# Optimization experiments

Measured on AMD Instinct MI355X. Metric: run time of the kernel, lower is better.

The kernel has to match this reference:

```python
import jax, jax.numpy as jnp
import numpy as np

D_MODEL = 192
NODE_NUM = 64
DEPTH = 2
ALPHA = 0.05
NUM_LAYERS = 2
LN_EPS = 1e-5


def _gcn(x, p):
    # x: [N, in_dim*D_MODEL]; faithful port of GCN.forward (eval mode)
    nv1, nv2, ws, bs, wm, bm, we, be, wl, bl, g, b = p
    N = x.shape[0]
    in_dim = x.shape[1] // D_MODEL
    adp = jax.nn.softmax(jax.nn.relu(nv1 @ nv2), axis=1)            # [V,V]
    adj = adp + jnp.eye(NODE_NUM, dtype=x.dtype)
    a = adj / adj.sum(1, keepdims=True)                              # row-normalized
    h0 = jax.lax.conv_general_dilated(
        x.reshape(N, in_dim, D_MODEL), ws, (1,), 'VALID',
        dimension_numbers=('NCH', 'OIH', 'NCH')) + bs[None, :, None]  # [N,C,V]
    h = h0
    outs = [h0]
    for _ in range(DEPTH):
        h = ALPHA * h0 + (1.0 - ALPHA) * jnp.einsum('ncw,vw->ncv', h, a)
        outs.append(h)
    ho = jnp.concatenate(outs, axis=1)                               # [N,(DEPTH+1)C,V]
    ho = jax.nn.gelu(jnp.einsum('ncv,oc->nov', ho, wm) + bm[None, :, None], approximate=False)
    ho = jnp.einsum('ncv,oc->nov', ho, we) + be[None, :, None]       # [N,6,V]
    ho = jnp.einsum('nov,dv->nod', ho, wl) + bl                      # [N,6,D]
    mu = ho.mean(-1, keepdims=True)
    var = ((ho - mu) ** 2).mean(-1, keepdims=True)                   # biased, like torch LN
    ho = (ho - mu) / jnp.sqrt(var + LN_EPS) * g + b
    return ho.reshape(N, 6 * D_MODEL)


def _encoder(inp4, flag, layer_params):
    x = jnp.transpose(inp4, (2, 0, 1, 3)) if flag == 1 else jnp.transpose(inp4, (1, 0, 2, 3))
    W, B, O, D = x.shape
    L = W + O - 1
    N = W * B
    # input_transfer: shift row r by r along the slice axis
    place = jax.vmap(lambda xr, r: jax.lax.dynamic_update_slice(
        jnp.zeros((B, L, D), x.dtype), xr, (0, r, 0)))
    a = place(x, jnp.arange(W)).reshape(N, L, D)
    layer0_output = None
    output_all = None
    rows_layers, cols_layers = [], []
    for layer in range(NUM_LAYERS):
        if layer >= 1:
            a = output_all  # eval mode: F.dropout is identity
            if layer == 1:
                layer0_output = a
        p = layer_params[layer]

        def step(carry, x_t, p=p):
            h_row, h_col = carry
            gate = _gcn(jnp.concatenate([h_row, h_col, x_t], axis=-1), p)  # [N,6D]
            sg = jax.nn.sigmoid(gate[:, :4 * D])
            tg = jnp.tanh(gate[:, 4 * D:])
            ug_r, og_r, ug_c, og_c = jnp.split(sg, 4, axis=-1)
            ig_r, ig_c = jnp.split(tg, 2, axis=-1)
            h_row = jnp.tanh((1.0 - ug_r) * h_row + ug_r * ig_r) * og_r
            h_col = jnp.tanh((1.0 - ug_c) * h_col + ug_c * ig_c) * og_c
            out_s = jnp.concatenate([h_row, h_col], axis=-1)
            # col hidden is saved pre-roll, rolled for next step
            return (h_row, jnp.roll(h_col, B, axis=0)), (out_s, h_row, h_col)

        init = (jnp.zeros((N, D), x.dtype), jnp.zeros((N, D), x.dtype))
        _, (outs, hrows, hcols) = jax.lax.scan(step, init, jnp.swapaxes(a, 0, 1))
        output_all = jnp.swapaxes(outs, 0, 1)                        # [N,L,2D]
        if layer >= 1:
            output_all = output_all + layer0_output
        # rows saved at slice s>=O-1 from block loc = s-O+1
        rows = hrows.reshape(L, W, B, D)[jnp.arange(O - 1, L), jnp.arange(W)]  # [W,B,D]
        # cols saved at slice s>=W-1 from last batch block
        cols = hcols[W - 1:, (W - 1) * B:, :]                        # [O,B,D]
        rows_layers.append(rows)
        cols_layers.append(cols)
    hidden_row_all = jnp.stack(rows_layers).transpose(2, 0, 1, 3)    # [B,layers,W,D]
    hidden_col_all = jnp.stack(cols_layers).transpose(2, 0, 1, 3)    # [B,layers,O,D]
    if flag == 1:
        return output_all, hidden_col_all, hidden_row_all
    return output_all, hidden_row_all, hidden_col_all


def setup_inputs() -> dict:
    key = jax.random.key(0)
    ks = jax.random.split(key, 20)
    idx = [0]
    def nxt():
        k = ks[idx[0]]
        idx[0] += 1
        return k
    B, W, O = 8, 24, 48
    K = D_MODEL - NODE_NUM + 1  # 129
    cc, sc, nd = 16, 32, 40
    d = {"input": jax.random.normal(nxt(), (B, W, O, D_MODEL), dtype=jnp.float32)}
    for li, in_dim in enumerate([3, 4]):
        d[f"nodevec1_{li}"] = jax.random.normal(nxt(), (NODE_NUM, nd), dtype=jnp.float32)
        d[f"nodevec2_{li}"] = jax.random.normal(nxt(), (nd, NODE_NUM), dtype=jnp.float32)
        d[f"w_start_{li}"] = jax.random.normal(nxt(), (cc, in_dim, K), dtype=jnp.float32) * 0.05
        d[f"b_start_{li}"] = jnp.zeros((cc,), jnp.float32)
        d[f"w_mlp_{li}"] = jax.random.normal(nxt(), (sc, (DEPTH + 1) * cc), dtype=jnp.float32) * 0.05
        d[f"b_mlp_{li}"] = jnp.zeros((sc,), jnp.float32)
        d[f"w_end_{li}"] = jax.random.normal(nxt(), (6, sc), dtype=jnp.float32) * 0.05
        d[f"b_end_{li}"] = jnp.zeros((6,), jnp.float32)
        d[f"w_lin_{li}"] = jax.random.normal(nxt(), (D_MODEL, NODE_NUM), dtype=jnp.float32) * 0.05
        d[f"b_lin_{li}"] = jnp.zeros((D_MODEL,), jnp.float32)
        d[f"gamma_{li}"] = jnp.ones((D_MODEL,), jnp.float32)
        d[f"beta_{li}"] = jnp.zeros((D_MODEL,), jnp.float32)
    d["flag"] = 0
    return d


def reference(input, nodevec1_0, nodevec2_0, w_start_0, b_start_0, w_mlp_0, b_mlp_0,
              w_end_0, b_end_0, w_lin_0, b_lin_0, gamma_0, beta_0,
              nodevec1_1, nodevec2_1, w_start_1, b_start_1, w_mlp_1, b_mlp_1,
              w_end_1, b_end_1, w_lin_1, b_lin_1, gamma_1, beta_1, flag):
    p0 = (nodevec1_0, nodevec2_0, w_start_0, b_start_0, w_mlp_0, b_mlp_0,
          w_end_0, b_end_0, w_lin_0, b_lin_0, gamma_0, beta_0)
    p1 = (nodevec1_1, nodevec2_1, w_start_1, b_start_1, w_mlp_1, b_mlp_1,
          w_end_1, b_end_1, w_lin_1, b_lin_1, gamma_1, beta_1)
    return _encoder(input, flag, (p0, p1))
```

## Files before the change

### kernel.cpp

```cpp
#include <hip/hip_runtime.h>
#include <hip/hip_bf16.h>

#define NT 512
typedef unsigned short u16;
typedef unsigned long long u64;

__device__ __forceinline__ u16 tobf(float x) {
  union { __hip_bfloat16 h; u16 u; } cv;
  cv.h = __float2bfloat16(x);
  return cv.u;
}
__device__ __forceinline__ float frombf(u16 u) {
  return __uint_as_float(((unsigned)u) << 16);
}
__device__ __forceinline__ float sigf(float x) {
  return __builtin_amdgcn_rcpf(1.f + __builtin_amdgcn_exp2f(-1.4426950408889634f * x));
}
__device__ __forceinline__ float tanh_fast(float x) {
  return 1.f - 2.f * __builtin_amdgcn_rcpf(1.f + __builtin_amdgcn_exp2f(2.8853900817779268f * x));
}
__device__ __forceinline__ void lds_fence() {
  asm volatile("s_waitcnt lgkmcnt(0)" ::: "memory");
  __builtin_amdgcn_sched_barrier(0);
}
__device__ __forceinline__ void bar_light() {
  asm volatile("s_waitcnt lgkmcnt(0)" ::: "memory");
  __builtin_amdgcn_s_barrier();
  asm volatile("" ::: "memory");
}

struct SeqArgs {
  const float* input;
  const float* nv1_0; const float* nv2_0; const float* nv1_1; const float* nv2_1;
  const float* w_start0; const float* b_start0; const float* w_mlp0; const float* b_mlp0;
  const float* w_end0;   const float* b_end0;   const float* w_lin0; const float* b_lin0;
  const float* gamma0;   const float* beta0;
  const float* w_start1; const float* b_start1; const float* w_mlp1; const float* b_mlp1;
  const float* w_end1;   const float* b_end1;   const float* w_lin1; const float* b_lin1;
  const float* gamma1;   const float* beta1;
  u64*   HCOL2;
  int*   prog;
  float* out_all; float* out_hrow; float* out_hcol;
};

__global__ __launch_bounds__(NT, 2) void seq_kernel(SeqArgs A) {
  const int n = blockIdx.x, w = n >> 3, b = n & 7, tid = threadIdx.x;
  const int pred = (n + 184) % 192;
  const int succ = (n + 8) % 192;

  __shared__ __align__(16) float sCIN[768];
  __shared__ __align__(16) u16   sWS[64 * 132];
  __shared__ __align__(16) float sATt[64 * 68];
  __shared__ __align__(16) float sH[2][1024];
  __shared__ __align__(16) float sHt[3 * 1280];
  __shared__ __align__(16) float sGt[64 * 44];
  __shared__ __align__(16) float sAbuf[4096];
  float* const sPart = sAbuf;
  float* const sE    = sAbuf + 2048;
  float* const sY    = sAbuf;
  float* const h0t   = sHt;
  float* const h1t   = sHt + 1280;
  float* const h2t   = sHt + 2560;

  for (int layer = 0; layer < 2; ++layer) {
    const int in_dim = 3 + layer;
    const int P = in_dim - 1;
    const float* nv1    = layer ? A.nv1_1    : A.nv1_0;
    const float* nv2    = layer ? A.nv2_1    : A.nv2_0;
    const float* wstart = layer ? A.w_start1 : A.w_start0;
    const float* bs     = layer ? A.b_start1 : A.b_start0;
    const float* wm     = layer ? A.w_mlp1   : A.w_mlp0;
    const float* bm     = layer ? A.b_mlp1   : A.b_mlp0;
    const float* we     = layer ? A.w_end1   : A.w_end0;
    const float* be     = layer ? A.b_end1   : A.b_end0;
    const float* wl     = layer ? A.w_lin1   : A.w_lin0;
    const float* bl     = layer ? A.b_lin1   : A.b_lin0;
    const float* gm     = layer ? A.gamma1   : A.gamma0;
    const float* bt     = layer ? A.beta1    : A.beta0;

    for (int idx = tid; idx < 4096; idx += NT) {
      int v = idx >> 6, ww = idx & 63;
      float s = 0.f;
      for (int j = 0; j < 40; ++j) s = fmaf(nv1[v*40 + j], nv2[j*64 + ww], s);
      sAbuf[idx] = fmaxf(s, 0.f);
    }
    __syncthreads();
    if (tid < 64) {
      const int v = tid;
      float m = -1e30f;
      for (int ww = 0; ww < 64; ++ww) m = fmaxf(m, sAbuf[v*64 + ww]);
      float s = 0.f;
      for (int ww = 0; ww < 64; ++ww) { float e = expf(sAbuf[v*64 + ww] - m); sAbuf[v*64 + ww] = e; s += e; }
      float inv = 1.f / s, rs = 1.f;
      for (int ww = 0; ww < 64; ++ww) rs += sAbuf[v*64 + ww] * inv;
      float irs = 1.f / rs;
      for (int ww = 0; ww < 64; ++ww) {
        float a = sAbuf[v*64 + ww] * inv + ((ww == v) ? 1.f : 0.f);
        sATt[v*68 + ww] = a * irs;
      }
    }
    __syncthreads();
    for (int idx = tid; idx < 16*in_dim*132; idx += NT) {
      int row = idx / 132, k = idx - row*132;
      sWS[idx] = (k < 129) ? tobf(wstart[((row & 15)*in_dim + (row >> 4))*129 + k]) : (u16)0;
    }
    for (int d = tid; d < 384; d += NT) sCIN[d] = 0.f;

    const int v_p = tid & 63;
    const int o0  = tid >> 6;
    const float bmv0 = bm[o0], bmv1 = bm[o0 + 8], bmv2 = bm[o0 + 16], bmv3 = bm[o0 + 24];
    float blv = 0.f, gmv = 1.f, btv = 0.f, bev = 0.f;
    if (tid < 384) { blv = bl[(tid >= 192) ? tid - 192 : tid]; bev = be[tid >> 6]; }
    if (tid < 192) { gmv = gm[tid]; btv = bt[tid]; }
    float bs_r[2];
    bs_r[0] = bs[tid >> 6];
    bs_r[1] = bs[(tid >> 6) + 8];
    __syncthreads();

    auto pre_conv = [&]() {
      const int nslots = P << 8;
      for (int s = tid; s < nslots; s += NT) {
        const int cidx = s >> 4;
        const int p = cidx >> 4, c = cidx & 15;
        const int vg = s & 15;
        const int ich = (p == 0) ? 0 : (p + 1);
        const float* xin = ((p == 0) ? &sCIN[0] : &sCIN[384 + (p-1)*192]) + vg*4;
        const u16* wrow = &sWS[(ich*16 + c)*132];
        float a0 = 0.f, a1 = 0.f, a2 = 0.f, a3 = 0.f;
        float4 xc = *(const float4*)xin;
        for (int k4 = 0; k4 < 128; k4 += 4) {
          ushort4 wu = *(const ushort4*)(wrow + k4);
          float w0 = frombf(wu.x), w1 = frombf(wu.y), w2 = frombf(wu.z), w3 = frombf(wu.w);
          float4 xn = *(const float4*)(xin + k4 + 4);
          a0 = fmaf(w3, xc.w, fmaf(w2, xc.z, fmaf(w1, xc.y, fmaf(w0, xc.x, a0))));
          a1 = fmaf(w3, xn.x, fmaf(w2, xc.w, fmaf(w1, xc.z, fmaf(w0, xc.y, a1))));
          a2 = fmaf(w3, xn.y, fmaf(w2, xn.x, fmaf(w1, xc.w, fmaf(w0, xc.z, a2))));
          a3 = fmaf(w3, xn.z, fmaf(w2, xn.y, fmaf(w1, xn.x, fmaf(w0, xc.w, a3))));
          xc = xn;
        }
        float wk = frombf(wrow[128]);
        a0 = fmaf(wk, xc.x, a0); a1 = fmaf(wk, xc.y, a1);
        a2 = fmaf(wk, xc.z, a2); a3 = fmaf(wk, xc.w, a3);
        *(float4*)&sPart[cidx*64 + vg*4] = make_float4(a0, a1, a2, a3);
      }
      bar_light();
      {
        const int c0 = tid >> 6, v = tid & 63;
        float sum0 = bs_r[0], sum1 = bs_r[1];
        for (int p = 0; p < P; ++p) {
          sum0 += sPart[(p*16 + c0     )*64 + v];
          sum1 += sPart[(p*16 + c0 + 8 )*64 + v];
        }
        sH[0][ c0      *64 + v] = sum0;
        sH[0][(c0 + 8 )*64 + v] = sum1;
      }
      bar_light();
    };

    {
      if (layer == 0) {
        int o = 0 - w;
        if (o >= 0 && o < 48) {
          const float* xr = A.input + (((size_t)(b*24 + w)*48 + o)*192);
          for (int d = tid; d < 192; d += NT) sCIN[384 + d] = xr[d];
        } else {
          for (int d = tid; d < 192; d += NT) sCIN[384 + d] = 0.f;
        }
      } else {
        const float* xr = A.out_all + ((size_t)n*71 + 0)*384;
        for (int d = tid; d < 384; d += NT) sCIN[384 + d] = xr[d];
      }
      bar_light();
      pre_conv();
    }

    for (int t = 0; t < 71; ++t) {
      const int S = layer*71 + t;

      float xpa = 0.f, xpb = 0.f;
      if (t < 70 && tid < 192) {
        if (layer == 0) {
          int o = (t + 1) - w;
          if (o >= 0 && o < 48)
            xpa = A.input[(((size_t)(b*24 + w)*48 + o)*192) + tid];
        } else {
          const float* xr = A.out_all + ((size_t)n*71 + (t+1))*384;
          xpa = xr[tid];
          xpb = xr[192 + tid];
        }
      }

      if (t > 0) {
        if (tid < 192) {
          const u64* src = &A.HCOL2[((size_t)((S-1) & 15)*192 + pred)*192 + tid];
          u64 v = __hip_atomic_load(src, __ATOMIC_RELAXED, __HIP_MEMORY_SCOPE_AGENT);
          while ((unsigned)(v >> 32) != (unsigned)S) {
            __builtin_amdgcn_s_sleep(1);
            v = __hip_atomic_load(src, __ATOMIC_RELAXED, __HIP_MEMORY_SCOPE_AGENT);
          }
          __builtin_amdgcn_sched_barrier(0);
          asm volatile("" ::: "memory");
          sCIN[192 + tid] = __uint_as_float((unsigned)v);
        } else if (tid == 256 && S >= 16) {
          while (__hip_atomic_load(&A.prog[succ*32], __ATOMIC_RELAXED, __HIP_MEMORY_SCOPE_AGENT) < S - 15)
            __builtin_amdgcn_s_sleep(2);
        }
        bar_light();
        if (tid == 0)
          __hip_atomic_store(&A.prog[n*32], S, __ATOMIC_RELAXED, __HIP_MEMORY_SCOPE_AGENT);
      } else if (S >= 16) {
        if (tid == 256) {
          while (__hip_atomic_load(&A.prog[succ*32], __ATOMIC_RELAXED, __HIP_MEMORY_SCOPE_AGENT) < S - 15)
            __builtin_amdgcn_s_sleep(2);
        }
      }

      if (tid < 256) {
        const int c = tid >> 4, vg = tid & 15;
        float4 acc = *(const float4*)&sH[0][c*64 + vg*4];
        float a0 = acc.x, a1 = acc.y, a2 = acc.z, a3 = acc.w;
        const u16* wrow = &sWS[(16 + c)*132];
        const float* xin = &sCIN[192 + vg*4];
        float4 xc = *(const float4*)xin;
        for (int k4 = 0; k4 < 128; k4 += 4) {
          ushort4 wu = *(const ushort4*)(wrow + k4);
          float w0 = frombf(wu.x), w1 = frombf(wu.y), w2 = frombf(wu.z), w3 = frombf(wu.w);
          float4 xn = *(const float4*)(xin + k4 + 4);
          a0 = fmaf(w3, xc.w, fmaf(w2, xc.z, fmaf(w1, xc.y, fmaf(w0, xc.x, a0))));
          a1 = fmaf(w3, xn.x, fmaf(w2, xc.w, fmaf(w1, xc.z, fmaf(w0, xc.y, a1))));
          a2 = fmaf(w3, xn.y, fmaf(w2, xn.x, fmaf(w1, xc.w, fmaf(w0, xc.z, a2))));
          a3 = fmaf(w3, xn.z, fmaf(w2, xn.y, fmaf(w1, xn.x, fmaf(w0, xc.w, a3))));
          xc = xn;
        }
        float wk = frombf(wrow[128]);
        a0 = fmaf(wk, xc.x, a0); a1 = fmaf(wk, xc.y, a1);
        a2 = fmaf(wk, xc.z, a2); a3 = fmaf(wk, xc.w, a3);
        *(float4*)&sH[0][c*64 + vg*4] = make_float4(a0, a1, a2, a3);
        const int v0 = vg*4;
        h0t[(v0    )*20 + c] = a0;
        h0t[(v0 + 1)*20 + c] = a1;
        h0t[(v0 + 2)*20 + c] = a2;
        h0t[(v0 + 3)*20 + c] = a3;
      }
      bar_light();

      {
        const int c0 = o0 * 2;
        float pa0 = 0.f, pa1 = 0.f;
        for (int w4 = 0; w4 < 64; w4 += 4) {
          float4 av = *(const float4*)&sATt[v_p*68 + w4];
          float4 h0v = *(const float4*)&sH[0][ c0      *64 + w4];
          float4 h1v = *(const float4*)&sH[0][(c0 + 1 )*64 + w4];
          pa0 = fmaf(h0v.x, av.x, pa0); pa0 = fmaf(h0v.y, av.y, pa0);
          pa0 = fmaf(h0v.z, av.z, pa0); pa0 = fmaf(h0v.w, av.w, pa0);
          pa1 = fmaf(h1v.x, av.x, pa1); pa1 = fmaf(h1v.y, av.y, pa1);
          pa1 = fmaf(h1v.z, av.z, pa1); pa1 = fmaf(h1v.w, av.w, pa1);
        }
        float h0a = sH[0][ c0      *64 + v_p];
        float h0b = sH[0][(c0 + 1 )*64 + v_p];
        float h1a = fmaf(0.95f, pa0, 0.05f * h0a);
        float h1b = fmaf(0.95f, pa1, 0.05f * h0b);
        sH[1][ c0      *64 + v_p] = h1a;
        sH[1][(c0 + 1 )*64 + v_p] = h1b;
        h1t[v_p*20 + c0    ] = h1a;
        h1t[v_p*20 + c0 + 1] = h1b;
        lds_fence();
        float pb0 = 0.f, pb1 = 0.f;
        for (int w4 = 0; w4 < 64; w4 += 4) {
          float4 av = *(const float4*)&sATt[v_p*68 + w4];
          float4 h0v = *(const float4*)&sH[1][ c0      *64 + w4];
          float4 h1v = *(const float4*)&sH[1][(c0 + 1 )*64 + w4];
          pb0 = fmaf(h0v.x, av.x, pb0); pb0 = fmaf(h0v.y, av.y, pb0);
          pb0 = fmaf(h0v.z, av.z, pb0); pb0 = fmaf(h0v.w, av.w, pb0);
          pb1 = fmaf(h1v.x, av.x, pb1); pb1 = fmaf(h1v.y, av.y, pb1);
          pb1 = fmaf(h1v.z, av.z, pb1); pb1 = fmaf(h1v.w, av.w, pb1);
        }
        h2t[v_p*20 + c0    ] = fmaf(0.95f, pb0, 0.05f * h0a);
        h2t[v_p*20 + c0 + 1] = fmaf(0.95f, pb1, 0.05f * h0b);
      }
      bar_light();

      {
        float g0 = bmv0, g1 = bmv1, g2 = bmv2, g3 = bmv3;
        const float* wr0 = wm + (o0     )*48;
        const float* wr1 = wm + (o0 +  8)*48;
        const float* wr2 = wm + (o0 + 16)*48;
        const float* wr3 = wm + (o0 + 24)*48;
        for (int cq = 0; cq < 4; ++cq) {
          float4 h0v = *(const float4*)&h0t[v_p*20 + cq*4];
          float4 h1v = *(const float4*)&h1t[v_p*20 + cq*4];
          float4 h2v = *(const float4*)&h2t[v_p*20 + cq*4];
          float4 wa0 = *(const float4*)(wr0 + cq*4);
          float4 wb0 = *(const float4*)(wr0 + 16 + cq*4);
          float4 wc0 = *(const float4*)(wr0 + 32 + cq*4);
          float4 wa1 = *(const float4*)(wr1 + cq*4);
          float4 wb1 = *(const float4*)(wr1 + 16 + cq*4);
          float4 wc1 = *(const float4*)(wr1 + 32 + cq*4);
          float4 wa2 = *(const float4*)(wr2 + cq*4);
          float4 wb2 = *(const float4*)(wr2 + 16 + cq*4);
          float4 wc2 = *(const float4*)(wr2 + 32 + cq*4);
          float4 wa3 = *(const float4*)(wr3 + cq*4);
          float4 wb3 = *(const float4*)(wr3 + 16 + cq*4);
          float4 wc3 = *(const float4*)(wr3 + 32 + cq*4);
          const float* h0p = (const float*)&h0v;
          const float* h1p = (const float*)&h1v;
          const float* h2p = (const float*)&h2v;
#pragma unroll
          for (int j = 0; j < 4; ++j) {
            float h0s = h0p[j], h1s = h1p[j], h2s = h2p[j];
            g0 = fmaf(((const float*)&wa0)[j], h0s, fmaf(((const float*)&wb0)[j], h1s, fmaf(((const float*)&wc0)[j], h2s, g0)));
            g1 = fmaf(((const float*)&wa1)[j], h0s, fmaf(((const float*)&wb1)[j], h1s, fmaf(((const float*)&wc1)[j], h2s, g1)));
            g2 = fmaf(((const float*)&wa2)[j], h0s, fmaf(((const float*)&wb2)[j], h1s, fmaf(((const float*)&wc2)[j], h2s, g2)));
            g3 = fmaf(((const float*)&wa3)[j], h0s, fmaf(((const float*)&wb3)[j], h1s, fmaf(((const float*)&wc3)[j], h2s, g3)));
          }
        }
        g0 = 0.5f * g0 * (1.f + erff(g0 * 0.70710678118654752f));
        g1 = 0.5f * g1 * (1.f + erff(g1 * 0.70710678118654752f));
        g2 = 0.5f * g2 * (1.f + erff(g2 * 0.70710678118654752f));
        g3 = 0.5f * g3 * (1.f + erff(g3 * 0.70710678118654752f));
        sGt[v_p*44 + o0     ] = g0;
        sGt[v_p*44 + o0 +  8] = g1;
        sGt[v_p*44 + o0 + 16] = g2;
        sGt[v_p*44 + o0 + 24] = g3;
      }
      bar_light();

      if (tid < 384) {
        const int o2 = tid >> 6, v = tid & 63;
        float acc = bev;
        const float* wer = we + o2*32;
        for (int c4 = 0; c4 < 8; ++c4) {
          float4 wev = *(const float4*)(wer + c4*4);
          float4 gv  = *(const float4*)&sGt[v*44 + c4*4];
          acc = fmaf(wev.x, gv.x, acc);
          acc = fmaf(wev.y, gv.y, acc);
          acc = fmaf(wev.z, gv.z, acc);
          acc = fmaf(wev.w, gv.w, acc);
        }
        sE[tid] = acc;
      }
      bar_light();

      if (tid < 384) {
        const int d  = (tid >= 192) ? tid - 192 : tid;
        const int r0 = (tid >= 192) ? 3 : 0;
        const float4* wrow = (const float4*)(wl + d*64);
        float y0 = blv, y1 = blv, y2 = blv;
        for (int q = 0; q < 16; ++q) {
          float4 wv = wrow[q];
          float4 e0 = *(const float4*)&sE[(r0+0)*64 + q*4];
          float4 e1 = *(const float4*)&sE[(r0+1)*64 + q*4];
          float4 e2 = *(const float4*)&sE[(r0+2)*64 + q*4];
          y0 = fmaf(e0.x,wv.x, fmaf(e0.y,wv.y, fmaf(e0.z,wv.z, fmaf(e0.w,wv.w, y0))));
          y1 = fmaf(e1.x,wv.x, fmaf(e1.y,wv.y, fmaf(e1.z,wv.z, fmaf(e1.w,wv.w, y1))));
          y2 = fmaf(e2.x,wv.x, fmaf(e2.y,wv.y, fmaf(e2.z,wv.z, fmaf(e2.w,wv.w, y2))));
        }
        sY[(r0+0)*192 + d] = y0;
        sY[(r0+1)*192 + d] = y1;
        sY[(r0+2)*192 + d] = y2;
      }
      bar_light();

      if (tid < 192) {
        const int r = tid >> 5, l32 = tid & 31;
        float sm = 0.f, sq = 0.f;
#pragma unroll
        for (int m = 0; m < 6; ++m) {
          float v = sY[r*192 + l32 + 32*m];
          sm += v; sq = fmaf(v, v, sq);
        }
#pragma unroll
        for (int off = 16; off >= 1; off >>= 1) {
          sm += __shfl_xor(sm, off);
          sq += __shfl_xor(sq, off);
        }
        if (l32 == 0) {
          float mu = sm * (1.f/192.f);
          float var = sq * (1.f/192.f) - mu*mu;
          sH[1][r] = mu;
          sH[1][8 + r] = rsqrtf(fmaxf(var, 0.f) + 1e-5f);
        }
      }
      bar_light();

      float hcn = 0.f;
      if (tid < 192) {
        const int d = tid;
        float y2 = fmaf((sY[2*192+d] - sH[1][2]) * sH[1][10], gmv, btv);
        float y3 = fmaf((sY[3*192+d] - sH[1][3]) * sH[1][11], gmv, btv);
        float y5 = fmaf((sY[5*192+d] - sH[1][5]) * sH[1][13], gmv, btv);
        float ugc = sigf(y2), ogc = sigf(y3), igc = tanh_fast(y5);
        float hc = sCIN[192 + d];
        hcn = tanh_fast(fmaf(ugc, igc, (1.f - ugc)*hc)) * ogc;
        u64 pk = ((u64)(unsigned)(S + 1) << 32) | (u64)__float_as_uint(hcn);
        __hip_atomic_store(&A.HCOL2[((size_t)(S & 15)*192 + n)*192 + d], pk,
                           __ATOMIC_RELAXED, __HIP_MEMORY_SCOPE_AGENT);
      }
      if (tid < 192) {
        const int d = tid;
        float y0 = fmaf((sY[0*192+d] - sH[1][0]) * sH[1][8],  gmv, btv);
        float y1 = fmaf((sY[1*192+d] - sH[1][1]) * sH[1][9],  gmv, btv);
        float y4 = fmaf((sY[4*192+d] - sH[1][4]) * sH[1][12], gmv, btv);
        float ugr = sigf(y0), ogr = sigf(y1), igr = tanh_fast(y4);
        float hr = sCIN[d];
        float hrn = tanh_fast(fmaf(ugr, igr, (1.f - ugr)*hr)) * ogr;
        sCIN[d] = hrn;
        float* oa = A.out_all + ((size_t)n*71 + t)*384;
        if (layer == 0) { oa[d] = hrn; oa[192 + d] = hcn; }
        else           { oa[d] = hrn + sCIN[384 + d]; oa[192 + d] = hcn + sCIN[576 + d]; }
        if (t == 47 + w)
          A.out_hrow[(((size_t)b*2 + layer)*24 + w)*192 + d] = hrn;
        if (w == 23 && t >= 23)
          A.out_hcol[(((size_t)b*2 + layer)*48 + (t - 23))*192 + d] = hcn;
        if (t < 70) {
          sCIN[384 + d] = xpa;
          if (layer == 1) sCIN[576 + d] = xpb;
        }
      }
      bar_light();
      if (t < 70) pre_conv();
    }
    __syncthreads();
  }
}

extern "C" void kernel_launch(void* const* d_in, const int* in_sizes, int n_in,
                              void* d_out, int out_size, void* d_ws, size_t ws_size,
                              hipStream_t stream) {
  (void)in_sizes; (void)n_in; (void)out_size; (void)ws_size;
  char* ws = (char*)d_ws;
  int* prog  = (int*)ws;
  u64* HCOL2 = (u64*)(ws + 24576);

  (void)hipMemsetAsync(ws, 0, 24576 + 4718592, stream);

  SeqArgs A;
  A.input    = (const float*)d_in[0];
  A.nv1_0    = (const float*)d_in[1];  A.nv2_0 = (const float*)d_in[2];
  A.w_start0 = (const float*)d_in[3];  A.b_start0 = (const float*)d_in[4];
  A.w_mlp0   = (const float*)d_in[5];  A.b_mlp0   = (const float*)d_in[6];
  A.w_end0   = (const float*)d_in[7];  A.b_end0   = (const float*)d_in[8];
  A.w_lin0   = (const float*)d_in[9];  A.b_lin0   = (const float*)d_in[10];
  A.gamma0   = (const float*)d_in[11]; A.beta0    = (const float*)d_in[12];
  A.nv1_1    = (const float*)d_in[13]; A.nv2_1 = (const float*)d_in[14];
  A.w_start1 = (const float*)d_in[15]; A.b_start1 = (const float*)d_in[16];
  A.w_mlp1   = (const float*)d_in[17]; A.b_mlp1   = (const float*)d_in[18];
  A.w_end1   = (const float*)d_in[19]; A.b_end1   = (const float*)d_in[20];
  A.w_lin1   = (const float*)d_in[21]; A.b_lin1   = (const float*)d_in[22];
  A.gamma1   = (const float*)d_in[23]; A.beta1    = (const float*)d_in[24];
  A.HCOL2 = HCOL2; A.prog = prog;
  A.out_all  = (float*)d_out;
  A.out_hrow = (float*)d_out + 5234688;
  A.out_hcol = (float*)d_out + 5308416;

  seq_kernel<<<192, NT, 0, stream>>>(A);
}
```

Baseline: 2.951 ms.

## Fuse conv tail with graph propagation and drop transposed LDS buffers

Result: slower. 3.164 ms (+7.2%).

```diff
diff --git a/kernel.cpp b/kernel.cpp
--- a/kernel.cpp
+++ b/kernel.cpp
@@ -52,15 +52,12 @@
   __shared__ __align__(16) u16   sWS[64 * 132];
   __shared__ __align__(16) float sATt[64 * 68];
   __shared__ __align__(16) float sH[2][1024];
-  __shared__ __align__(16) float sHt[3 * 1280];
-  __shared__ __align__(16) float sGt[64 * 44];
-  __shared__ __align__(16) float sAbuf[4096];
+  __shared__ __align__(16) float sAbuf[4928];
   float* const sPart = sAbuf;
+  float* const sG    = sAbuf;
+  float* const sH2c  = sAbuf + 2048;
   float* const sE    = sAbuf + 2048;
   float* const sY    = sAbuf;
-  float* const h0t   = sHt;
-  float* const h1t   = sHt + 1280;
-  float* const h2t   = sHt + 2560;
 
   for (int layer = 0; layer < 2; ++layer) {
     const int in_dim = 3 + layer;
@@ -115,6 +112,8 @@
     float bs_r[2];
     bs_r[0] = bs[tid >> 6];
     bs_r[1] = bs[(tid >> 6) + 8];
+    const float* wmS = wm + __builtin_amdgcn_readfirstlane(o0) * 48;
+    const float* weS = we + __builtin_amdgcn_readfirstlane((tid < 384) ? (tid >> 6) : 0) * 32;
     __syncthreads();
 
     auto pre_conv = [&]() {
@@ -217,126 +216,93 @@
 
       if (tid < 256) {
         const int c = tid >> 4, vg = tid & 15;
-        float4 acc = *(const float4*)&sH[0][c*64 + vg*4];
-        float a0 = acc.x, a1 = acc.y, a2 = acc.z, a3 = acc.w;
-        const u16* wrow = &sWS[(16 + c)*132];
-        const float* xin = &sCIN[192 + vg*4];
-        float4 xc = *(const float4*)xin;
-        for (int k4 = 0; k4 < 128; k4 += 4) {
-          ushort4 wu = *(const ushort4*)(wrow + k4);
-          float w0 = frombf(wu.x), w1 = frombf(wu.y), w2 = frombf(wu.z), w3 = frombf(wu.w);
-          float4 xn = *(const float4*)(xin + k4 + 4);
-          a0 = fmaf(w3, xc.w, fmaf(w2, xc.z, fmaf(w1, xc.y, fmaf(w0, xc.x, a0))));
-          a1 = fmaf(w3, xn.x, fmaf(w2, xc.w, fmaf(w1, xc.z, fmaf(w0, xc.y, a1))));
-          a2 = fmaf(w3, xn.y, fmaf(w2, xn.x, fmaf(w1, xc.w, fmaf(w0, xc.z, a2))));
-          a3 = fmaf(w3, xn.z, fmaf(w2, xn.y, fmaf(w1, xn.x, fmaf(w0, xc.w, a3))));
-          xc = xn;
-        }
-        float wk = frombf(wrow[128]);
-        a0 = fmaf(wk, xc.x, a0); a1 = fmaf(wk, xc.y, a1);
-        a2 = fmaf(wk, xc.z, a2); a3 = fmaf(wk, xc.w, a3);
-        *(float4*)&sH[0][c*64 + vg*4] = make_float4(a0, a1, a2, a3);
-        const int v0 = vg*4;
-        h0t[(v0    )*20 + c] = a0;
-        h0t[(v0 + 1)*20 + c] = a1;
-        h0t[(v0 + 2)*20 + c] = a2;
-        h0t[(v0 + 3)*20 + c] = a3;
-      }
-      bar_light();
-
-      {
-        const int c0 = o0 * 2;
-        float pa0 = 0.f, pa1 = 0.f;
+        {
+          float4 acc = *(const float4*)&sH[0][c*64 + vg*4];
+          float a0 = acc.x, a1 = acc.y, a2 = acc.z, a3 = acc.w;
+          const u16* wrow = &sWS[(16 + c)*132];
+          const float* xin = &sCIN[192 + vg*4];
+          float4 xc = *(const float4*)xin;
+          for (int k4 = 0; k4 < 128; k4 += 4) {
+            ushort4 wu = *(const ushort4*)(wrow + k4);
+            float w0 = frombf(wu.x), w1 = frombf(wu.y), w2 = frombf(wu.z), w3 = frombf(wu.w);
+            float4 xn = *(const float4*)(xin + k4 + 4);
+            a0 = fmaf(w3, xc.w, fmaf(w2, xc.z, fmaf(w1, xc.y, fmaf(w0, xc.x, a0))));
+            a1 = fmaf(w3, xn.x, fmaf(w2, xc.w, fmaf(w1, xc.z, fmaf(w0, xc.y, a1))));
+            a2 = fmaf(w3, xn.y, fmaf(w2, xn.x, fmaf(w1, xc.w, fmaf(w0, xc.z, a2))));
+            a3 = fmaf(w3, xn.z, fmaf(w2, xn.y, fmaf(w1, xn.x, fmaf(w0, xc.w, a3))));
+            xc = xn;
+          }
+          float wk = frombf(wrow[128]);
+          a0 = fmaf(wk, xc.x, a0); a1 = fmaf(wk, xc.y, a1);
+          a2 = fmaf(wk, xc.z, a2); a3 = fmaf(wk, xc.w, a3);
+          *(float4*)&sH[0][c*64 + vg*4] = make_float4(a0, a1, a2, a3);
+        }
+        lds_fence();
+        const int r0 = (tid >> 6) * 4;
+        float h0a[4];
+#pragma unroll
+        for (int j = 0; j < 4; ++j) h0a[j] = sH[0][(r0+j)*64 + v_p];
+        float pa[4] = {0.f, 0.f, 0.f, 0.f};
         for (int w4 = 0; w4 < 64; w4 += 4) {
           float4 av = *(const float4*)&sATt[v_p*68 + w4];
-          float4 h0v = *(const float4*)&sH[0][ c0      *64 + w4];
-          float4 h1v = *(const float4*)&sH[0][(c0 + 1 )*64 + w4];
-          pa0 = fmaf(h0v.x, av.x, pa0); pa0 = fmaf(h0v.y, av.y, pa0);
-          pa0 = fmaf(h0v.z, av.z, pa0); pa0 = fmaf(h0v.w, av.w, pa0);
-          pa1 = fmaf(h1v.x, av.x, pa1); pa1 = fmaf(h1v.y, av.y, pa1);
-          pa1 = fmaf(h1v.z, av.z, pa1); pa1 = fmaf(h1v.w, av.w, pa1);
-        }
-        float h0a = sH[0][ c0      *64 + v_p];
-        float h0b = sH[0][(c0 + 1 )*64 + v_p];
-        float h1a = fmaf(0.95f, pa0, 0.05f * h0a);
-        float h1b = fmaf(0.95f, pa1, 0.05f * h0b);
-        sH[1][ c0      *64 + v_p] = h1a;
-        sH[1][(c0 + 1 )*64 + v_p] = h1b;
-        h1t[v_p*20 + c0    ] = h1a;
-        h1t[v_p*20 + c0 + 1] = h1b;
+#pragma unroll
+          for (int j = 0; j < 4; ++j) {
+            float4 hv = *(const float4*)&sH[0][(r0+j)*64 + w4];
+            pa[j] = fmaf(hv.x, av.x, pa[j]); pa[j] = fmaf(hv.y, av.y, pa[j]);
+            pa[j] = fmaf(hv.z, av.z, pa[j]); pa[j] = fmaf(hv.w, av.w, pa[j]);
+          }
+        }
+#pragma unroll
+        for (int j = 0; j < 4; ++j)
+          sH[1][(r0+j)*64 + v_p] = fmaf(0.95f, pa[j], 0.05f * h0a[j]);
         lds_fence();
-        float pb0 = 0.f, pb1 = 0.f;
+        float pb[4] = {0.f, 0.f, 0.f, 0.f};
         for (int w4 = 0; w4 < 64; w4 += 4) {
           float4 av = *(const float4*)&sATt[v_p*68 + w4];
-          float4 h0v = *(const float4*)&sH[1][ c0      *64 + w4];
-          float4 h1v = *(const float4*)&sH[1][(c0 + 1 )*64 + w4];
-          pb0 = fmaf(h0v.x, av.x, pb0); pb0 = fmaf(h0v.y, av.y, pb0);
-          pb0 = fmaf(h0v.z, av.z, pb0); pb0 = fmaf(h0v.w, av.w, pb0);
-          pb1 = fmaf(h1v.x, av.x, pb1); pb1 = fmaf(h1v.y, av.y, pb1);
-          pb1 = fmaf(h1v.z, av.z, pb1); pb1 = fmaf(h1v.w, av.w, pb1);
-        }
-        h2t[v_p*20 + c0    ] = fmaf(0.95f, pb0, 0.05f * h0a);
-        h2t[v_p*20 + c0 + 1] = fmaf(0.95f, pb1, 0.05f * h0b);
+#pragma unroll
+          for (int j = 0; j < 4; ++j) {
+            float4 hv = *(const float4*)&sH[1][(r0+j)*64 + w4];
+            pb[j] = fmaf(hv.x, av.x, pb[j]); pb[j] = fmaf(hv.y, av.y, pb[j]);
+            pb[j] = fmaf(hv.z, av.z, pb[j]); pb[j] = fmaf(hv.w, av.w, pb[j]);
+          }
+        }
+#pragma unroll
+        for (int j = 0; j < 4; ++j)
+          sH2c[(r0+j)*64 + v_p] = fmaf(0.95f, pb[j], 0.05f * h0a[j]);
       }
       bar_light();
 
       {
         float g0 = bmv0, g1 = bmv1, g2 = bmv2, g3 = bmv3;
-        const float* wr0 = wm + (o0     )*48;
-        const float* wr1 = wm + (o0 +  8)*48;
-        const float* wr2 = wm + (o0 + 16)*48;
-        const float* wr3 = wm + (o0 + 24)*48;
-        for (int cq = 0; cq < 4; ++cq) {
-          float4 h0v = *(const float4*)&h0t[v_p*20 + cq*4];
-          float4 h1v = *(const float4*)&h1t[v_p*20 + cq*4];
-          float4 h2v = *(const float4*)&h2t[v_p*20 + cq*4];
-          float4 wa0 = *(const float4*)(wr0 + cq*4);
-          float4 wb0 = *(const float4*)(wr0 + 16 + cq*4);
-          float4 wc0 = *(const float4*)(wr0 + 32 + cq*4);
-          float4 wa1 = *(const float4*)(wr1 + cq*4);
-          float4 wb1 = *(const float4*)(wr1 + 16 + cq*4);
-          float4 wc1 = *(const float4*)(wr1 + 32 + cq*4);
-          float4 wa2 = *(const float4*)(wr2 + cq*4);
-          float4 wb2 = *(const float4*)(wr2 + 16 + cq*4);
-          float4 wc2 = *(const float4*)(wr2 + 32 + cq*4);
-          float4 wa3 = *(const float4*)(wr3 + cq*4);
-          float4 wb3 = *(const float4*)(wr3 + 16 + cq*4);
-          float4 wc3 = *(const float4*)(wr3 + 32 + cq*4);
-          const float* h0p = (const float*)&h0v;
-          const float* h1p = (const float*)&h1v;
-          const float* h2p = (const float*)&h2v;
-#pragma unroll
-          for (int j = 0; j < 4; ++j) {
-            float h0s = h0p[j], h1s = h1p[j], h2s = h2p[j];
-            g0 = fmaf(((const float*)&wa0)[j], h0s, fmaf(((const float*)&wb0)[j], h1s, fmaf(((const float*)&wc0)[j], h2s, g0)));
-            g1 = fmaf(((const float*)&wa1)[j], h0s, fmaf(((const float*)&wb1)[j], h1s, fmaf(((const float*)&wc1)[j], h2s, g1)));
-            g2 = fmaf(((const float*)&wa2)[j], h0s, fmaf(((const float*)&wb2)[j], h1s, fmaf(((const float*)&wc2)[j], h2s, g2)));
-            g3 = fmaf(((const float*)&wa3)[j], h0s, fmaf(((const float*)&wb3)[j], h1s, fmaf(((const float*)&wc3)[j], h2s, g3)));
-          }
+        const float* wr0 = wmS;
+        const float* wr1 = wmS + 8*48;
+        const float* wr2 = wmS + 16*48;
+        const float* wr3 = wmS + 24*48;
+#pragma unroll
+        for (int c = 0; c < 16; ++c) {
+          float h0v = sH[0][c*64 + v_p];
+          float h1v = sH[1][c*64 + v_p];
+          float h2v = sH2c[c*64 + v_p];
+          g0 = fmaf(wr0[c], h0v, fmaf(wr0[16 + c], h1v, fmaf(wr0[32 + c], h2v, g0)));
+          g1 = fmaf(wr1[c], h0v, fmaf(wr1[16 + c], h1v, fmaf(wr1[32 + c], h2v, g1)));
+          g2 = fmaf(wr2[c], h0v, fmaf(wr2[16 + c], h1v, fmaf(wr2[32 + c], h2v, g2)));
+          g3 = fmaf(wr3[c], h0v, fmaf(wr3[16 + c], h1v, fmaf(wr3[32 + c], h2v, g3)));
         }
         g0 = 0.5f * g0 * (1.f + erff(g0 * 0.70710678118654752f));
         g1 = 0.5f * g1 * (1.f + erff(g1 * 0.70710678118654752f));
         g2 = 0.5f * g2 * (1.f + erff(g2 * 0.70710678118654752f));
         g3 = 0.5f * g3 * (1.f + erff(g3 * 0.70710678118654752f));
-        sGt[v_p*44 + o0     ] = g0;
-        sGt[v_p*44 + o0 +  8] = g1;
-        sGt[v_p*44 + o0 + 16] = g2;
-        sGt[v_p*44 + o0 + 24] = g3;
+        sG[(o0     )*64 + v_p] = g0;
+        sG[(o0 +  8)*64 + v_p] = g1;
+        sG[(o0 + 16)*64 + v_p] = g2;
+        sG[(o0 + 24)*64 + v_p] = g3;
       }
       bar_light();
 
       if (tid < 384) {
-        const int o2 = tid >> 6, v = tid & 63;
+        const int v = tid & 63;
         float acc = bev;
-        const float* wer = we + o2*32;
-        for (int c4 = 0; c4 < 8; ++c4) {
-          float4 wev = *(const float4*)(wer + c4*4);
-          float4 gv  = *(const float4*)&sGt[v*44 + c4*4];
-          acc = fmaf(wev.x, gv.x, acc);
-          acc = fmaf(wev.y, gv.y, acc);
-          acc = fmaf(wev.z, gv.z, acc);
-          acc = fmaf(wev.w, gv.w, acc);
-        }
+        for (int c = 0; c < 32; ++c) acc = fmaf(weS[c], sG[c*64 + v], acc);
         sE[tid] = acc;
       }
       bar_light();
```
